# Optimization experiments

Hardware: AMD Instinct MI355X
Metric: run time of the kernel (lower is better)

The kernel has to match this reference:

```python
import jax, jax.numpy as jnp
import numpy as np

E, B, DX, DC, DH, DO = 16, 4096, 128, 64, 1024, 128
DIN = DX + DC

def setup_inputs() -> dict:
    key = jax.random.key(0)
    ks = jax.random.split(key, 6)
    s1 = 1.0 / np.sqrt(DIN)
    s2 = 1.0 / np.sqrt(DH)
    return {
        "x": jax.random.normal(ks[0], (E, B, DX), dtype=jnp.float32),
        "cond": jax.random.normal(ks[1], (E, B, DC), dtype=jnp.float32),
        # stacked per-expert params, mirroring param_stacks ([E, ...])
        "W1": jax.random.uniform(ks[2], (E, DH, DIN), minval=-s1, maxval=s1, dtype=jnp.float32),
        "b1": jax.random.uniform(ks[3], (E, DH), minval=-s1, maxval=s1, dtype=jnp.float32),
        "W2": jax.random.uniform(ks[4], (E, DO, DH), minval=-s2, maxval=s2, dtype=jnp.float32),
        "b2": jax.random.uniform(ks[5], (E, DO), minval=-s2, maxval=s2, dtype=jnp.float32),
    }

def reference(x, cond, W1, b1, W2, b2):
    # vmap over experts == grouped GEMM with per-expert weight tiles
    xc = jnp.concatenate([x, cond], axis=-1)          # [E, B, DIN]
    h = jnp.einsum('ebi,ehi->ebh', xc, W1) + b1[:, None, :]  # [E, B, DH]
    h = jax.nn.relu(h)
    y = jnp.einsum('ebh,eoh->ebo', h, W2) + b2[:, None, :]   # [E, B, DO]
    return y
```

## Files before the change

kernel.cpp:

```cpp
#include <hip/hip_runtime.h>
#include <hip/hip_bf16.h>

#define E_   16
#define B_   4096
#define DX_  128
#define DC_  64
#define DIN_ 192
#define DH_  1024
#define DO_  128

#define BM 256
#define KC 64
#define NCHUNK (DH_ / KC)
#define NT 512

typedef __attribute__((ext_vector_type(4))) float f32x4;
typedef __attribute__((ext_vector_type(8))) short bf16x8;

__device__ __forceinline__ unsigned f2bf_u(float f) {
    union { float f; unsigned u; } v; v.f = f;
    return (v.u + 0x7fffu + ((v.u >> 16) & 1u)) >> 16;
}
__device__ __forceinline__ uint2 pack4(float4 v) {
    uint2 r;
    r.x = f2bf_u(v.x) | (f2bf_u(v.y) << 16);
    r.y = f2bf_u(v.z) | (f2bf_u(v.w) << 16);
    return r;
}
__device__ __forceinline__ int swz(int r, int S, int cb) {
    return r * S + ((cb ^ ((r & 7) << 4)) >> 1);
}

__global__ __launch_bounds__(NT, 2)
void moe_fused_kernel(const float* __restrict__ x, const float* __restrict__ cond,
                      const float* __restrict__ W1, const float* __restrict__ b1,
                      const float* __restrict__ W2, const float* __restrict__ b2,
                      float* __restrict__ out) {
    __shared__ short XCs[BM * DIN_];
    __shared__ short WB [KC * DIN_];
    __shared__ short HB [BM * KC];

    const int bid = blockIdx.x;
    const int xcd = bid & 7;
    const int s   = bid >> 3;
    const int e   = 2 * xcd + (s & 1);
    const int row0 = (s >> 1) * BM;

    const int tid  = threadIdx.x;
    const int w    = tid >> 6;
    const int lane = tid & 63;
    const int lr   = lane & 15;
    const int lg   = lane >> 4;

    const float4* g1base = (const float4*)(W1 + (size_t)e * DH_ * DIN_);

    float4 r1[6];
#pragma unroll
    for (int i = 0; i < 6; ++i) r1[i] = g1base[tid + NT * i];

    {
        const float4* gx = (const float4*)(x + (size_t)(e * B_ + row0) * DX_);
#pragma unroll
        for (int i = 0; i < 16; ++i) {
            int g = tid + NT * i;
            int r = g >> 5, c = g & 31;
            *(uint2*)&XCs[swz(r, DIN_, c * 8)] = pack4(gx[g]);
        }
        const float4* gc = (const float4*)(cond + (size_t)(e * B_ + row0) * DC_);
#pragma unroll
        for (int i = 0; i < 8; ++i) {
            int g = tid + NT * i;
            int r = g >> 4, c = g & 15;
            *(uint2*)&XCs[128 + swz(r, DIN_, c * 8)] = pack4(gc[g]);
        }
    }

    f32x4 acc2[4][4] = {};

    for (int c = 0; c < NCHUNK; ++c) {
        __syncthreads();

#pragma unroll
        for (int i = 0; i < 6; ++i) {
            int g = tid + NT * i;
            int r = g / 48, cc = g - r * 48;
            *(uint2*)&WB[swz(r, DIN_, cc * 8)] = pack4(r1[i]);
        }
        __syncthreads();

        float4 r2[4];
        {
            const float* g2 = W2 + (size_t)e * DO_ * DH_ + (size_t)c * KC;
#pragma unroll
            for (int i = 0; i < 4; ++i) {
                int g = tid + NT * i;
                int r = g >> 4, cc = g & 15;
                r2[i] = *(const float4*)(g2 + (size_t)r * DH_ + cc * 4);
            }
        }
        float b1v[4];
#pragma unroll
        for (int nf = 0; nf < 4; ++nf)
            b1v[nf] = b1[e * DH_ + c * KC + nf * 16 + lr];

        const int band = w * 32;
        f32x4 acc1[2][4] = {};
#pragma unroll
        for (int kk = 0; kk < DIN_ / 32; ++kk) {
            bf16x8 af[2], bfr[4];
#pragma unroll
            for (int mf = 0; mf < 2; ++mf) {
                int r = band + mf * 16 + lr;
                af[mf] = *(const bf16x8*)&XCs[swz(r, DIN_, kk * 64 + lg * 16)];
            }
#pragma unroll
            for (int nf = 0; nf < 4; ++nf) {
                int r = nf * 16 + lr;
                bfr[nf] = *(const bf16x8*)&WB[swz(r, DIN_, kk * 64 + lg * 16)];
            }
#pragma unroll
            for (int mf = 0; mf < 2; ++mf)
#pragma unroll
                for (int nf = 0; nf < 4; ++nf)
                    acc1[mf][nf] = __builtin_amdgcn_mfma_f32_16x16x32_bf16(af[mf], bfr[nf], acc1[mf][nf], 0, 0, 0);
        }
#pragma unroll
        for (int mf = 0; mf < 2; ++mf)
#pragma unroll
            for (int nf = 0; nf < 4; ++nf)
#pragma unroll
                for (int j = 0; j < 4; ++j) {
                    float v = fmaxf(acc1[mf][nf][j] + b1v[nf], 0.f);
                    int hr = band + mf * 16 + lg * 4 + j;
                    int hc = nf * 16 + lr;
                    HB[swz(hr, KC, 2 * hc)] = (short)f2bf_u(v);
                }
        __syncthreads();

#pragma unroll
        for (int i = 0; i < 4; ++i) {
            int g = tid + NT * i;
            int r = g >> 4, cc = g & 15;
            *(uint2*)&WB[swz(r, KC, cc * 8)] = pack4(r2[i]);
        }
        __syncthreads();

        if (c + 1 < NCHUNK) {
#pragma unroll
            for (int i = 0; i < 6; ++i)
                r1[i] = g1base[(c + 1) * (KC * DIN_ / 4) + tid + NT * i];
        }

        const int wr = w >> 1, wc2 = w & 1;
#pragma unroll
        for (int kk = 0; kk < KC / 32; ++kk) {
            bf16x8 af[4], bfr[4];
#pragma unroll
            for (int mf = 0; mf < 4; ++mf) {
                int r = wr * 64 + mf * 16 + lr;
                af[mf] = *(const bf16x8*)&HB[swz(r, KC, kk * 64 + lg * 16)];
            }
#pragma unroll
            for (int nf = 0; nf < 4; ++nf) {
                int r = wc2 * 64 + nf * 16 + lr;
                bfr[nf] = *(const bf16x8*)&WB[swz(r, KC, kk * 64 + lg * 16)];
            }
#pragma unroll
            for (int mf = 0; mf < 4; ++mf)
#pragma unroll
                for (int nf = 0; nf < 4; ++nf)
                    acc2[mf][nf] = __builtin_amdgcn_mfma_f32_16x16x32_bf16(af[mf], bfr[nf], acc2[mf][nf], 0, 0, 0);
        }
    }

    const int wr = w >> 1, wc2 = w & 1;
    float b2v[4];
#pragma unroll
    for (int nf = 0; nf < 4; ++nf)
        b2v[nf] = b2[e * DO_ + wc2 * 64 + nf * 16 + lr];
#pragma unroll
    for (int mf = 0; mf < 4; ++mf)
#pragma unroll
        for (int nf = 0; nf < 4; ++nf)
#pragma unroll
            for (int j = 0; j < 4; ++j) {
                int m = wr * 64 + mf * 16 + lg * 4 + j;
                int o = wc2 * 64 + nf * 16 + lr;
                out[(size_t)(e * B_ + row0 + m) * DO_ + o] = acc2[mf][nf][j] + b2v[nf];
            }
}

extern "C" void kernel_launch(void* const* d_in, const int* in_sizes, int n_in,
                              void* d_out, int out_size, void* d_ws, size_t ws_size,
                              hipStream_t stream) {
    const float* x    = (const float*)d_in[0];
    const float* cond = (const float*)d_in[1];
    const float* W1   = (const float*)d_in[2];
    const float* b1   = (const float*)d_in[3];
    const float* W2   = (const float*)d_in[4];
    const float* b2   = (const float*)d_in[5];
    float* out = (float*)d_out;

    dim3 grid(E_ * (B_ / BM));
    dim3 block(NT);
    moe_fused_kernel<<<grid, block, 0, stream>>>(x, cond, W1, b1, W2, b2, out);
}
```

Before: 164.5 us.

## Double-buffer weight/hidden tiles and software-pipeline GEMM2 behind GEMM1

Replaces the three separate shared arrays with one union buffer. The concatenated x/cond tile now lives in registers for the whole loop, which frees shared memory for double-buffered W1, W2 and hidden tiles. Each iteration runs GEMM2 on the previous chunk while GEMM1 works on the current one, and next-chunk global loads are issued two steps ahead. This cuts the barriers per chunk from four to one. In exchange it uses more registers (twelve extra bf16x8 operands held under a 2-block launch bound), which risks spills or lower occupancy.

```diff
diff --git a/kernel.cpp b/kernel.cpp
--- a/kernel.cpp
+++ b/kernel.cpp
@@ -14,6 +14,13 @@
 #define NCHUNK (DH_ / KC)
 #define NT 512
 
+#define W1B_OFF 0
+#define W1B_STR 12288
+#define W2B_OFF 24576
+#define W2B_STR 8192
+#define HB_OFF  40960
+#define HB_STR  16384
+
 typedef __attribute__((ext_vector_type(4))) float f32x4;
 typedef __attribute__((ext_vector_type(8))) short bf16x8;
 
@@ -36,9 +43,7 @@
                       const float* __restrict__ W1, const float* __restrict__ b1,
                       const float* __restrict__ W2, const float* __restrict__ b2,
                       float* __restrict__ out) {
-    __shared__ short XCs[BM * DIN_];
-    __shared__ short WB [KC * DIN_];
-    __shared__ short HB [BM * KC];
+    __shared__ short LDSU[73728];
 
     const int bid = blockIdx.x;
     const int xcd = bid & 7;
@@ -51,6 +56,8 @@
     const int lane = tid & 63;
     const int lr   = lane & 15;
     const int lg   = lane >> 4;
+    const int band = w * 32;
+    const int wr   = w >> 1, wc2 = w & 1;
 
     const float4* g1base = (const float4*)(W1 + (size_t)e * DH_ * DIN_);
 
@@ -64,33 +71,78 @@
         for (int i = 0; i < 16; ++i) {
             int g = tid + NT * i;
             int r = g >> 5, c = g & 31;
-            *(uint2*)&XCs[swz(r, DIN_, c * 8)] = pack4(gx[g]);
+            *(uint2*)&LDSU[swz(r, DIN_, c * 8)] = pack4(gx[g]);
         }
         const float4* gc = (const float4*)(cond + (size_t)(e * B_ + row0) * DC_);
 #pragma unroll
         for (int i = 0; i < 8; ++i) {
             int g = tid + NT * i;
             int r = g >> 4, c = g & 15;
-            *(uint2*)&XCs[128 + swz(r, DIN_, c * 8)] = pack4(gc[g]);
-        }
-    }
+            *(uint2*)&LDSU[128 + swz(r, DIN_, c * 8)] = pack4(gc[g]);
+        }
+    }
+    __syncthreads();
+
+    bf16x8 xcreg[2][6];
+#pragma unroll
+    for (int mf = 0; mf < 2; ++mf)
+#pragma unroll
+        for (int kk = 0; kk < 6; ++kk)
+            xcreg[mf][kk] = *(const bf16x8*)&LDSU[swz(band + mf * 16 + lr, DIN_, kk * 64 + lg * 16)];
+    __syncthreads();
+
+#pragma unroll
+    for (int i = 0; i < 6; ++i) {
+        int g = tid + NT * i;
+        int r = g / 48, cc = g - r * 48;
+        *(uint2*)&LDSU[W1B_OFF + swz(r, DIN_, cc * 8)] = pack4(r1[i]);
+    }
+#pragma unroll
+    for (int i = 0; i < 6; ++i)
+        r1[i] = g1base[(KC * DIN_ / 4) + tid + NT * i];
+    float4 r2[4];
+    {
+        const float* g2 = W2 + (size_t)e * DO_ * DH_;
+#pragma unroll
+        for (int i = 0; i < 4; ++i) {
+            int g = tid + NT * i;
+            int r = g >> 4, cc = g & 15;
+            r2[i] = *(const float4*)(g2 + (size_t)r * DH_ + cc * 4);
+        }
+    }
+    __syncthreads();
 
     f32x4 acc2[4][4] = {};
 
     for (int c = 0; c < NCHUNK; ++c) {
-        __syncthreads();
-
-#pragma unroll
-        for (int i = 0; i < 6; ++i) {
-            int g = tid + NT * i;
-            int r = g / 48, cc = g - r * 48;
-            *(uint2*)&WB[swz(r, DIN_, cc * 8)] = pack4(r1[i]);
-        }
-        __syncthreads();
-
-        float4 r2[4];
-        {
-            const float* g2 = W2 + (size_t)e * DO_ * DH_ + (size_t)c * KC;
+        const int pc = c & 1, pp = pc ^ 1;
+
+        float b1v[4];
+#pragma unroll
+        for (int nf = 0; nf < 4; ++nf)
+            b1v[nf] = b1[e * DH_ + c * KC + nf * 16 + lr];
+
+#pragma unroll
+        for (int i = 0; i < 4; ++i) {
+            int g = tid + NT * i;
+            int r = g >> 4, cc = g & 15;
+            *(uint2*)&LDSU[W2B_OFF + pc * W2B_STR + swz(r, KC, cc * 8)] = pack4(r2[i]);
+        }
+        if (c + 1 < NCHUNK) {
+#pragma unroll
+            for (int i = 0; i < 6; ++i) {
+                int g = tid + NT * i;
+                int r = g / 48, cc = g - r * 48;
+                *(uint2*)&LDSU[W1B_OFF + pp * W1B_STR + swz(r, DIN_, cc * 8)] = pack4(r1[i]);
+            }
+        }
+        if (c + 2 < NCHUNK) {
+#pragma unroll
+            for (int i = 0; i < 6; ++i)
+                r1[i] = g1base[(c + 2) * (KC * DIN_ / 4) + tid + NT * i];
+        }
+        if (c + 1 < NCHUNK) {
+            const float* g2 = W2 + (size_t)e * DO_ * DH_ + (size_t)(c + 1) * KC;
 #pragma unroll
             for (int i = 0; i < 4; ++i) {
                 int g = tid + NT * i;
@@ -98,31 +150,43 @@
                 r2[i] = *(const float4*)(g2 + (size_t)r * DH_ + cc * 4);
             }
         }
-        float b1v[4];
-#pragma unroll
-        for (int nf = 0; nf < 4; ++nf)
-            b1v[nf] = b1[e * DH_ + c * KC + nf * 16 + lr];
-
-        const int band = w * 32;
+
+        if (c > 0) {
+#pragma unroll
+            for (int kk = 0; kk < KC / 32; ++kk) {
+                bf16x8 af[4], bfr[4];
+#pragma unroll
+                for (int mf = 0; mf < 4; ++mf) {
+                    int r = wr * 64 + mf * 16 + lr;
+                    af[mf] = *(const bf16x8*)&LDSU[HB_OFF + pp * HB_STR + swz(r, KC, kk * 64 + lg * 16)];
+                }
+#pragma unroll
+                for (int nf = 0; nf < 4; ++nf) {
+                    int r = wc2 * 64 + nf * 16 + lr;
+                    bfr[nf] = *(const bf16x8*)&LDSU[W2B_OFF + pp * W2B_STR + swz(r, KC, kk * 64 + lg * 16)];
+                }
+#pragma unroll
+                for (int mf = 0; mf < 4; ++mf)
+#pragma unroll
+                    for (int nf = 0; nf < 4; ++nf)
+                        acc2[mf][nf] = __builtin_amdgcn_mfma_f32_16x16x32_bf16(af[mf], bfr[nf], acc2[mf][nf], 0, 0, 0);
+            }
+        }
+
         f32x4 acc1[2][4] = {};
 #pragma unroll
         for (int kk = 0; kk < DIN_ / 32; ++kk) {
-            bf16x8 af[2], bfr[4];
-#pragma unroll
-            for (int mf = 0; mf < 2; ++mf) {
-                int r = band + mf * 16 + lr;
-                af[mf] = *(const bf16x8*)&XCs[swz(r, DIN_, kk * 64 + lg * 16)];
-            }
+            bf16x8 bfr[4];
 #pragma unroll
             for (int nf = 0; nf < 4; ++nf) {
                 int r = nf * 16 + lr;
-                bfr[nf] = *(const bf16x8*)&WB[swz(r, DIN_, kk * 64 + lg * 16)];
+                bfr[nf] = *(const bf16x8*)&LDSU[W1B_OFF + pc * W1B_STR + swz(r, DIN_, kk * 64 + lg * 16)];
             }
 #pragma unroll
             for (int mf = 0; mf < 2; ++mf)
 #pragma unroll
                 for (int nf = 0; nf < 4; ++nf)
-                    acc1[mf][nf] = __builtin_amdgcn_mfma_f32_16x16x32_bf16(af[mf], bfr[nf], acc1[mf][nf], 0, 0, 0);
+                    acc1[mf][nf] = __builtin_amdgcn_mfma_f32_16x16x32_bf16(xcreg[mf][kk], bfr[nf], acc1[mf][nf], 0, 0, 0);
         }
 #pragma unroll
         for (int mf = 0; mf < 2; ++mf)
@@ -133,37 +197,26 @@
                     float v = fmaxf(acc1[mf][nf][j] + b1v[nf], 0.f);
                     int hr = band + mf * 16 + lg * 4 + j;
                     int hc = nf * 16 + lr;
-                    HB[swz(hr, KC, 2 * hc)] = (short)f2bf_u(v);
+                    LDSU[HB_OFF + pc * HB_STR + swz(hr, KC, 2 * hc)] = (short)f2bf_u(v);
                 }
+
         __syncthreads();
-
-#pragma unroll
-        for (int i = 0; i < 4; ++i) {
-            int g = tid + NT * i;
-            int r = g >> 4, cc = g & 15;
-            *(uint2*)&WB[swz(r, KC, cc * 8)] = pack4(r2[i]);
-        }
-        __syncthreads();
-
-        if (c + 1 < NCHUNK) {
-#pragma unroll
-            for (int i = 0; i < 6; ++i)
-                r1[i] = g1base[(c + 1) * (KC * DIN_ / 4) + tid + NT * i];
-        }
-
-        const int wr = w >> 1, wc2 = w & 1;
+    }
+
+    {
+        const int pl = (NCHUNK - 1) & 1;
 #pragma unroll
         for (int kk = 0; kk < KC / 32; ++kk) {
             bf16x8 af[4], bfr[4];
 #pragma unroll
             for (int mf = 0; mf < 4; ++mf) {
                 int r = wr * 64 + mf * 16 + lr;
-                af[mf] = *(const bf16x8*)&HB[swz(r, KC, kk * 64 + lg * 16)];
+                af[mf] = *(const bf16x8*)&LDSU[HB_OFF + pl * HB_STR + swz(r, KC, kk * 64 + lg * 16)];
             }
 #pragma unroll
             for (int nf = 0; nf < 4; ++nf) {
                 int r = wc2 * 64 + nf * 16 + lr;
-                bfr[nf] = *(const bf16x8*)&WB[swz(r, KC, kk * 64 + lg * 16)];
+                bfr[nf] = *(const bf16x8*)&LDSU[W2B_OFF + pl * W2B_STR + swz(r, KC, kk * 64 + lg * 16)];
             }
 #pragma unroll
             for (int mf = 0; mf < 4; ++mf)
@@ -173,7 +226,6 @@
         }
     }
 
-    const int wr = w >> 1, wc2 = w & 1;
     float b2v[4];
 #pragma unroll
     for (int nf = 0; nf < 4; ++nf)
```

Result: slower. 193.0 us (+17.3%).
